# Performance work log

Measured on AMD Instinct MI355X. Metric: run time of the kernel, lower is better.

Reference implementation:

```python
import jax, jax.numpy as jnp
import numpy as np

T = 2048
V = 1024
H = 2048


def setup_inputs() -> dict:
    key = jax.random.key(0)
    ks = jax.random.split(key, 7)
    s_in = 1.0 / np.sqrt(V + H)
    s_out = 1.0 / np.sqrt(2 * H)
    return {
        "Wf_w": jax.random.normal(ks[0], (4 * H, V + H), jnp.float32) * s_in,
        "Wf_b": jnp.zeros((4 * H,), jnp.float32),
        "Wb_w": jax.random.normal(ks[1], (4 * H, V + H), jnp.float32) * s_in,
        "Wb_b": jnp.zeros((4 * H,), jnp.float32),
        "Wo_w": jax.random.normal(ks[2], (V, 2 * H), jnp.float32) * s_out,
        "Wo_b": jnp.zeros((V,), jnp.float32),
        "char_idx": jax.random.randint(ks[3], (T,), 0, V, jnp.int32),
    }


def _lstm_scan(x_seq, W, b, reverse):
    # x_seq: [T, V]; W: [4H, V+H]; b: [4H]
    h0 = jnp.zeros((H,), x_seq.dtype)
    c0 = jnp.zeros((H,), x_seq.dtype)

    def step(carry, xt):
        h, c = carry
        gates = jnp.concatenate([xt, h]) @ W.T + b  # [4H]
        i, f, g, o = jnp.split(gates, 4)
        i = jax.nn.sigmoid(i)
        f = jax.nn.sigmoid(f)
        o = jax.nn.sigmoid(o)
        g = jnp.tanh(g)
        c_new = f * c + i * g
        h_new = o * jnp.tanh(c_new)
        return (h_new, c_new), h_new

    _, hs = jax.lax.scan(step, (h0, c0), x_seq, reverse=reverse)
    return hs  # [T, H], aligned with input time order


def reference(Wf_w, Wf_b, Wb_w, Wb_b, Wo_w, Wo_b, char_idx):
    x = jax.nn.one_hot(char_idx, V, dtype=Wf_w.dtype)  # [T, V]
    hf = _lstm_scan(x, Wf_w, Wf_b, reverse=False)      # forward states
    hb = _lstm_scan(x, Wb_w, Wb_b, reverse=True)       # backward states
    merged = jnp.concatenate([hf, hb], axis=-1)         # [T, 2H]
    out = merged @ Wo_w.T + Wo_b                        # [T, V]
    return out
```

## Files before the change

### kernel.cpp

```cpp
#include <hip/hip_runtime.h>
#include <math.h>

#define TT 2048
#define VV 1024
#define HH 2048
#define SS (VV + HH)

#define NWGD 128
#define BTH  512
#define UPW  16
#define KSL  32
#define KPT  64

#define HL2W 68
#define HL2SZ (KSL * HL2W)

static_assert(NWGD * UPW == HH, "unit coverage");
static_assert(UPW * KSL == BTH, "thread coverage");
static_assert(KSL * KPT == HH, "k coverage");

typedef _Float16 half2_t __attribute__((ext_vector_type(2)));
typedef unsigned uint4v  __attribute__((ext_vector_type(4)));

#if defined(__has_builtin)
#if __has_builtin(__builtin_amdgcn_fdot2)
#define FDOT2(w, h, c) __builtin_amdgcn_fdot2((w), (h), (c), false)
#endif
#endif
#ifndef FDOT2
__device__ __forceinline__ float fdot2_asm(half2_t w, half2_t h, float c) {
    float r = c;
    asm volatile("v_dot2_f32_f16 %0, %1, %2, %0" : "+v"(r) : "v"(w), "v"(h));
    return r;
}
#define FDOT2(w, h, c) fdot2_asm((w), (h), (c))
#endif

__device__ __forceinline__ float sigmoidf_(float x) {
    return 1.0f / (1.0f + __expf(-x));
}

#define LDS_BARRIER() asm volatile("s_waitcnt lgkmcnt(0)\n\ts_barrier" ::: "memory")


__global__ __launch_bounds__(BTH) __attribute__((amdgpu_waves_per_eu(2, 2)))
void lstm_kernel(const float* __restrict__ Wf, const float* __restrict__ bfv,
                 const float* __restrict__ Wb, const float* __restrict__ bbv,
                 const int* __restrict__ cidx,
                 float* __restrict__ hsf, float* __restrict__ hsb,
                 unsigned* __restrict__ mbx)
{
    const int wg   = blockIdx.x;
    const int dir  = wg >> 7;
    const int w    = wg & (NWGD - 1);
    const int tid  = threadIdx.x;
    const int rg   = tid >> 5;
    const int ks   = tid & (KSL - 1);
    const int unit = w * UPW + rg;

    const float* W    = dir ? Wb : Wf;
    const float* bias = dir ? bbv : bfv;
    float* hs         = dir ? hsb : hsf;
    unsigned* mbd     = mbx + (size_t)dir * (2 * NWGD * 16);

    __shared__ unsigned long long hl2_u64[2 * HL2SZ / 4];
    __shared__ unsigned hstage[UPW];
    __shared__ char force_one_wg[100 * 1024];
    if (tid == 0) ((volatile char*)force_one_wg)[0] = 0;
    ushort* hl2 = (ushort*)hl2_u64;

    half2_t w2[4][KPT / 2];
    #pragma unroll
    for (int j = 0; j < 4; ++j) {
        const float* rbase = W + (size_t)(j * HH + unit) * SS + VV + ks * KPT;
        #pragma unroll
        for (int q = 0; q < KPT / 4; ++q) {
            const float4 wv = *reinterpret_cast<const float4*>(rbase + 4 * q);
            w2[j][2 * q]     = half2_t{(_Float16)wv.x, (_Float16)wv.y};
            w2[j][2 * q + 1] = half2_t{(_Float16)wv.z, (_Float16)wv.w};
        }
    }
    const float b_i = bias[0 * HH + unit];
    const float b_f = bias[1 * HH + unit];
    const float b_g = bias[2 * HH + unit];
    const float b_o = bias[3 * HH + unit];
    float creg = 0.0f;

    for (int i = tid; i < HL2SZ / 4; i += BTH) hl2_u64[i] = 0ull;
    if (tid < UPW) hstage[tid] = 0u;

    float gx0 = 0.f, gx1 = 0.f, gx2 = 0.f, gx3 = 0.f;
    if (ks == 0) {
        const int xt0 = cidx[dir ? (TT - 1) : 0];
        gx0 = W[(size_t)(0 * HH + unit) * SS + xt0];
        gx1 = W[(size_t)(1 * HH + unit) * SS + xt0];
        gx2 = W[(size_t)(2 * HH + unit) * SS + xt0];
        gx3 = W[(size_t)(3 * HH + unit) * SS + xt0];
    }
    __syncthreads();

    for (int s = 0; s < TT; ++s) {
        const int t = dir ? (TT - 1 - s) : s;

        float a0 = 0.f, a1 = 0.f, a2 = 0.f, a3 = 0.f;
        const ushort* hrow = hl2 + (s & 1) * HL2SZ + ks * HL2W;
        #pragma unroll
        for (int c = 0; c < KPT / 4; ++c) {
            const unsigned long long hv8 =
                *reinterpret_cast<const unsigned long long*>(hrow + c * 4);
            const half2_t ha = __builtin_bit_cast(half2_t, (unsigned)hv8);
            const half2_t hc = __builtin_bit_cast(half2_t, (unsigned)(hv8 >> 32));
            a0 = FDOT2(w2[0][2 * c], ha, a0); a0 = FDOT2(w2[0][2 * c + 1], hc, a0);
            a1 = FDOT2(w2[1][2 * c], ha, a1); a1 = FDOT2(w2[1][2 * c + 1], hc, a1);
            a2 = FDOT2(w2[2][2 * c], ha, a2); a2 = FDOT2(w2[2][2 * c + 1], hc, a2);
            a3 = FDOT2(w2[3][2 * c], ha, a3); a3 = FDOT2(w2[3][2 * c + 1], hc, a3);
        }

        float sA = (ks & 1) ? a0 : a1, kA = (ks & 1) ? a1 : a0;
        float A  = kA + __shfl_xor(sA, 1, 64);
        float sB = (ks & 1) ? a2 : a3, kB = (ks & 1) ? a3 : a2;
        float B  = kB + __shfl_xor(sB, 1, 64);
        float sC = (ks & 2) ? A : B,  kC = (ks & 2) ? B : A;
        float C  = kC + __shfl_xor(sC, 2, 64);
        C += __shfl_xor(C, 4, 64);
        C += __shfl_xor(C, 8, 64);
        C += __shfl_xor(C, 16, 64);
        const float Cf = __shfl(C, 1, 32);
        const float Cg = __shfl(C, 2, 32);
        const float Co = __shfl(C, 3, 32);

        if (ks == 0) {
            const float gi = sigmoidf_(C  + gx0 + b_i);
            const float gf = sigmoidf_(Cf + gx1 + b_f);
            const float gg = tanhf(Cg + gx2 + b_g);
            const float go = sigmoidf_(Co + gx3 + b_o);
            creg = gf * creg + gi * gg;
            const float hv = go * tanhf(creg);
            hs[(size_t)t * HH + unit] = hv;
            const unsigned hbits =
                (unsigned)__builtin_bit_cast(ushort, (_Float16)hv);
            ((volatile unsigned*)hstage)[rg] = ((unsigned)(s + 1) << 16) | hbits;
        }

        if (tid < 4) {
            const unsigned tg = ((unsigned)(s + 1)) << 16;
            volatile unsigned* hp = hstage + 4 * tid;
            unsigned x0, x1, x2, x3;
            for (;;) {
                x0 = hp[0]; x1 = hp[1]; x2 = hp[2]; x3 = hp[3];
                if ((((x0 ^ tg) | (x1 ^ tg) | (x2 ^ tg) | (x3 ^ tg))
                     & 0xFFFF0000u) == 0u) break;
            }
            const uint4v pv = {(x0 & 0xFFFFu) | (x1 << 16),
                               (x2 & 0xFFFFu) | (x3 << 16),
                               0u, (unsigned)(s + 1)};
            unsigned* dst = mbd + (size_t)(s & 1) * (NWGD * 16) + w * 16 + tid * 4;
            asm volatile("global_store_dwordx4 %0, %1, off sc0 sc1"
                         :: "v"(dst), "v"(pv) : "memory");
        }

        if (s + 1 < TT) {
            const unsigned tag = (unsigned)(s + 1);
            const unsigned* src = mbd + (size_t)(s & 1) * (NWGD * 16)
                                + (tid >> 2) * 16 + (tid & 3) * 4;
            uint4v v;
            for (;;) {
                asm volatile("global_load_dwordx4 %0, %1, off sc0 sc1\n\t"
                             "s_waitcnt vmcnt(0)"
                             : "=&v"(v) : "v"(src) : "memory");
                if (v.w == tag) break;
                __builtin_amdgcn_s_sleep(1);
            }
            const unsigned long long hv8 =
                (unsigned long long)v.x | ((unsigned long long)v.y << 32);

            if (ks == 0) {
                const int xtn = cidx[dir ? (t - 1) : (t + 1)];
                gx0 = W[(size_t)(0 * HH + unit) * SS + xtn];
                gx1 = W[(size_t)(1 * HH + unit) * SS + xtn];
                gx2 = W[(size_t)(2 * HH + unit) * SS + xtn];
                gx3 = W[(size_t)(3 * HH + unit) * SS + xtn];
            }

            *reinterpret_cast<unsigned long long*>(
                hl2 + ((s + 1) & 1) * HL2SZ + (tid >> 4) * HL2W + (tid & 15) * 4)
                = hv8;

            LDS_BARRIER();
        }
    }
}

__global__ __launch_bounds__(256)
void out_gemm(const float* __restrict__ hsf, const float* __restrict__ hsb,
              const float* __restrict__ Wo, const float* __restrict__ bo,
              float* __restrict__ out)
{
    const int bn = blockIdx.x;
    const int bm = blockIdx.y;
    const int tid = threadIdx.x;
    const int tx = tid & 15, ty = tid >> 4;
    const int t0 = bm * 64, v0 = bn * 64;

    __shared__ float As[32][72];
    __shared__ float Bs[32][72];

    float acc[4][4] = {};

    const int rr = tid >> 2;
    const int kc = tid & 3;

    for (int kb = 0; kb < 2 * HH; kb += 32) {
        {
            const int k = kb + kc * 8;
            const float* asrc = (k < HH) ? (hsf + (size_t)(t0 + rr) * HH + k)
                                         : (hsb + (size_t)(t0 + rr) * HH + (k - HH));
            const float4 a0 = *reinterpret_cast<const float4*>(asrc);
            const float4 a1 = *reinterpret_cast<const float4*>(asrc + 4);
            const int kk = kc * 8;
            As[kk+0][rr]=a0.x; As[kk+1][rr]=a0.y; As[kk+2][rr]=a0.z; As[kk+3][rr]=a0.w;
            As[kk+4][rr]=a1.x; As[kk+5][rr]=a1.y; As[kk+6][rr]=a1.z; As[kk+7][rr]=a1.w;
            const float* bsrc = Wo + (size_t)(v0 + rr) * (2 * HH) + k;
            const float4 b0 = *reinterpret_cast<const float4*>(bsrc);
            const float4 b1 = *reinterpret_cast<const float4*>(bsrc + 4);
            Bs[kk+0][rr]=b0.x; Bs[kk+1][rr]=b0.y; Bs[kk+2][rr]=b0.z; Bs[kk+3][rr]=b0.w;
            Bs[kk+4][rr]=b1.x; Bs[kk+5][rr]=b1.y; Bs[kk+6][rr]=b1.z; Bs[kk+7][rr]=b1.w;
        }
        __syncthreads();
        #pragma unroll 8
        for (int kk = 0; kk < 32; ++kk) {
            const float4 av = *reinterpret_cast<const float4*>(&As[kk][ty * 4]);
            const float4 bv = *reinterpret_cast<const float4*>(&Bs[kk][tx * 4]);
            const float a[4] = {av.x, av.y, av.z, av.w};
            const float b[4] = {bv.x, bv.y, bv.z, bv.w};
            #pragma unroll
            for (int i2 = 0; i2 < 4; ++i2)
                #pragma unroll
                for (int j2 = 0; j2 < 4; ++j2)
                    acc[i2][j2] = fmaf(a[i2], b[j2], acc[i2][j2]);
        }
        __syncthreads();
    }
    #pragma unroll
    for (int i2 = 0; i2 < 4; ++i2) {
        const int t = t0 + ty * 4 + i2;
        #pragma unroll
        for (int j2 = 0; j2 < 4; ++j2) {
            const int v = v0 + tx * 4 + j2;
            out[(size_t)t * VV + v] = acc[i2][j2] + bo[v];
        }
    }
}

extern "C" void kernel_launch(void* const* d_in, const int* in_sizes, int n_in,
                              void* d_out, int out_size, void* d_ws, size_t ws_size,
                              hipStream_t stream)
{
    (void)in_sizes; (void)n_in; (void)out_size; (void)ws_size;

    const float* Wf  = (const float*)d_in[0];
    const float* bfv = (const float*)d_in[1];
    const float* Wb  = (const float*)d_in[2];
    const float* bbv = (const float*)d_in[3];
    const float* Wo  = (const float*)d_in[4];
    const float* bo  = (const float*)d_in[5];
    const int*   cid = (const int*)d_in[6];
    float* out = (float*)d_out;

    unsigned char* ws = (unsigned char*)d_ws;
    unsigned* mbx = (unsigned*)ws;
    float* hsf = (float*)(ws + 65536);
    float* hsb = hsf + (size_t)TT * HH;

    (void)hipMemsetAsync(mbx, 0, 32768, stream);

    lstm_kernel<<<dim3(2 * NWGD), dim3(BTH), 0, stream>>>(Wf, bfv, Wb, bbv, cid,
                                                          hsf, hsb, mbx);
    out_gemm<<<dim3(VV / 64, TT / 64), dim3(256), 0, stream>>>(hsf, hsb, Wo, bo, out);
}
```

Baseline: 5.763 ms.

## Replicate per-step hidden-state mailbox and store fp16 hidden history from one workgroup

Each workgroup now publishes its hidden-state slice to 16 replicated mailbox copies, and readers poll the copy chosen by their index. This spreads the polling traffic that all 128 workgroups of a direction previously aimed at one buffer, which should shorten the per-step cross-workgroup exchange. The hidden-state history is now stored as fp16, written once per step by a single rotating workgroup from the mailbox data instead of scattered fp32 stores by every unit. The output GEMM reads and converts this fp16 history, which halves its activation traffic but lowers the precision of its input.

Result: slower. 6.244 ms (+8.4%).

```diff
diff --git a/kernel.cpp b/kernel.cpp
--- a/kernel.cpp
+++ b/kernel.cpp
@@ -11,6 +11,9 @@
 #define UPW  16
 #define KSL  32
 #define KPT  64
+
+#define NREP 16
+#define MB_PAR (NREP * NWGD * 16)
 
 #define HL2W 68
 #define HL2SZ (KSL * HL2W)
@@ -40,6 +43,10 @@
     return 1.0f / (1.0f + __expf(-x));
 }
 
+__device__ __forceinline__ float h2f(unsigned u) {
+    return (float)__builtin_bit_cast(_Float16, (unsigned short)(u & 0xFFFFu));
+}
+
 #define LDS_BARRIER() asm volatile("s_waitcnt lgkmcnt(0)\n\ts_barrier" ::: "memory")
 
 
@@ -47,7 +54,7 @@
 void lstm_kernel(const float* __restrict__ Wf, const float* __restrict__ bfv,
                  const float* __restrict__ Wb, const float* __restrict__ bbv,
                  const int* __restrict__ cidx,
-                 float* __restrict__ hsf, float* __restrict__ hsb,
+                 ushort* __restrict__ hs16f, ushort* __restrict__ hs16b,
                  unsigned* __restrict__ mbx)
 {
     const int wg   = blockIdx.x;
@@ -60,8 +67,8 @@
 
     const float* W    = dir ? Wb : Wf;
     const float* bias = dir ? bbv : bfv;
-    float* hs         = dir ? hsb : hsf;
-    unsigned* mbd     = mbx + (size_t)dir * (2 * NWGD * 16);
+    ushort* hs16      = dir ? hs16b : hs16f;
+    unsigned* mbd     = mbx + (size_t)dir * 2 * MB_PAR;
 
     __shared__ unsigned long long hl2_u64[2 * HL2SZ / 4];
     __shared__ unsigned hstage[UPW];
@@ -136,15 +143,14 @@
             const float go = sigmoidf_(Co + gx3 + b_o);
             creg = gf * creg + gi * gg;
             const float hv = go * tanhf(creg);
-            hs[(size_t)t * HH + unit] = hv;
             const unsigned hbits =
                 (unsigned)__builtin_bit_cast(ushort, (_Float16)hv);
             ((volatile unsigned*)hstage)[rg] = ((unsigned)(s + 1) << 16) | hbits;
         }
 
-        if (tid < 4) {
+        if (tid < 64) {
             const unsigned tg = ((unsigned)(s + 1)) << 16;
-            volatile unsigned* hp = hstage + 4 * tid;
+            volatile unsigned* hp = hstage + 4 * (tid & 3);
             unsigned x0, x1, x2, x3;
             for (;;) {
                 x0 = hp[0]; x1 = hp[1]; x2 = hp[2]; x3 = hp[3];
@@ -154,14 +160,16 @@
             const uint4v pv = {(x0 & 0xFFFFu) | (x1 << 16),
                                (x2 & 0xFFFFu) | (x3 << 16),
                                0u, (unsigned)(s + 1)};
-            unsigned* dst = mbd + (size_t)(s & 1) * (NWGD * 16) + w * 16 + tid * 4;
+            unsigned* dst = mbd + (size_t)(s & 1) * MB_PAR
+                          + (tid >> 2) * (NWGD * 16) + w * 16 + (tid & 3) * 4;
             asm volatile("global_store_dwordx4 %0, %1, off sc0 sc1"
                          :: "v"(dst), "v"(pv) : "memory");
         }
 
-        if (s + 1 < TT) {
+        {
             const unsigned tag = (unsigned)(s + 1);
-            const unsigned* src = mbd + (size_t)(s & 1) * (NWGD * 16)
+            const unsigned* src = mbd + (size_t)(s & 1) * MB_PAR
+                                + (w & (NREP - 1)) * (NWGD * 16)
                                 + (tid >> 2) * 16 + (tid & 3) * 4;
             uint4v v;
             for (;;) {
@@ -174,25 +182,30 @@
             const unsigned long long hv8 =
                 (unsigned long long)v.x | ((unsigned long long)v.y << 32);
 
-            if (ks == 0) {
-                const int xtn = cidx[dir ? (t - 1) : (t + 1)];
-                gx0 = W[(size_t)(0 * HH + unit) * SS + xtn];
-                gx1 = W[(size_t)(1 * HH + unit) * SS + xtn];
-                gx2 = W[(size_t)(2 * HH + unit) * SS + xtn];
-                gx3 = W[(size_t)(3 * HH + unit) * SS + xtn];
+            if (w == (s & (NWGD - 1)))
+                *reinterpret_cast<unsigned long long*>(
+                    hs16 + (size_t)t * HH + 4 * tid) = hv8;
+
+            if (s + 1 < TT) {
+                if (ks == 0) {
+                    const int xtn = cidx[dir ? (t - 1) : (t + 1)];
+                    gx0 = W[(size_t)(0 * HH + unit) * SS + xtn];
+                    gx1 = W[(size_t)(1 * HH + unit) * SS + xtn];
+                    gx2 = W[(size_t)(2 * HH + unit) * SS + xtn];
+                    gx3 = W[(size_t)(3 * HH + unit) * SS + xtn];
+                }
+                *reinterpret_cast<unsigned long long*>(
+                    hl2 + ((s + 1) & 1) * HL2SZ + (tid >> 4) * HL2W
+                        + (tid & 15) * 4) = hv8;
+                LDS_BARRIER();
             }
-
-            *reinterpret_cast<unsigned long long*>(
-                hl2 + ((s + 1) & 1) * HL2SZ + (tid >> 4) * HL2W + (tid & 15) * 4)
-                = hv8;
-
-            LDS_BARRIER();
-        }
-    }
+        }
+    }
+    asm volatile("s_waitcnt vmcnt(0) lgkmcnt(0)" ::: "memory");
 }
 
 __global__ __launch_bounds__(256)
-void out_gemm(const float* __restrict__ hsf, const float* __restrict__ hsb,
+void out_gemm(const ushort* __restrict__ hs16f, const ushort* __restrict__ hs16b,
               const float* __restrict__ Wo, const float* __restrict__ bo,
               float* __restrict__ out)
 {
@@ -213,13 +226,15 @@
     for (int kb = 0; kb < 2 * HH; kb += 32) {
         {
             const int k = kb + kc * 8;
-            const float* asrc = (k < HH) ? (hsf + (size_t)(t0 + rr) * HH + k)
-                                         : (hsb + (size_t)(t0 + rr) * HH + (k - HH));
-            const float4 a0 = *reinterpret_cast<const float4*>(asrc);
-            const float4 a1 = *reinterpret_cast<const float4*>(asrc + 4);
+            const ushort* asrc = (k < HH)
+                ? (hs16f + (size_t)(t0 + rr) * HH + k)
+                : (hs16b + (size_t)(t0 + rr) * HH + (k - HH));
+            const uint4v av = *reinterpret_cast<const uint4v*>(asrc);
             const int kk = kc * 8;
-            As[kk+0][rr]=a0.x; As[kk+1][rr]=a0.y; As[kk+2][rr]=a0.z; As[kk+3][rr]=a0.w;
-            As[kk+4][rr]=a1.x; As[kk+5][rr]=a1.y; As[kk+6][rr]=a1.z; As[kk+7][rr]=a1.w;
+            As[kk+0][rr]=h2f(av.x); As[kk+1][rr]=h2f(av.x>>16);
+            As[kk+2][rr]=h2f(av.y); As[kk+3][rr]=h2f(av.y>>16);
+            As[kk+4][rr]=h2f(av.z); As[kk+5][rr]=h2f(av.z>>16);
+            As[kk+6][rr]=h2f(av.w); As[kk+7][rr]=h2f(av.w>>16);
             const float* bsrc = Wo + (size_t)(v0 + rr) * (2 * HH) + k;
             const float4 b0 = *reinterpret_cast<const float4*>(bsrc);
             const float4 b1 = *reinterpret_cast<const float4*>(bsrc + 4);
@@ -269,12 +284,13 @@
 
     unsigned char* ws = (unsigned char*)d_ws;
     unsigned* mbx = (unsigned*)ws;
-    float* hsf = (float*)(ws + 65536);
-    float* hsb = hsf + (size_t)TT * HH;
-
-    (void)hipMemsetAsync(mbx, 0, 32768, stream);
+    ushort* hs16f = (ushort*)(ws + (1 << 20));
+    ushort* hs16b = hs16f + (size_t)TT * HH;
+
+    (void)hipMemsetAsync(mbx, 0, 2 * 2 * MB_PAR * 4, stream);
 
     lstm_kernel<<<dim3(2 * NWGD), dim3(BTH), 0, stream>>>(Wf, bfv, Wb, bbv, cid,
-                                                          hsf, hsb, mbx);
-    out_gemm<<<dim3(VV / 64, TT / 64), dim3(256), 0, stream>>>(hsf, hsb, Wo, bo, out);
-}
+                                                          hs16f, hs16b, mbx);
+    out_gemm<<<dim3(VV / 64, TT / 64), dim3(256), 0, stream>>>(hs16f, hs16b,
+                                                               Wo, bo, out);
+}
```
